# Kernel optimization log

Measured on AMD Instinct MI355X. Metric: run time of the kernel, lower is better.

The kernel has to match this reference:

```python
import jax, jax.numpy as jnp
import numpy as np

EPS = 1e-4
IN_DIM, D1, D2 = 30, 20, 15


def _orthogonal(key, rows, cols):
    # mimic nn.init.orthogonal_ for a (rows, cols) matrix with rows < cols
    a = jax.random.normal(key, (cols, rows), dtype=jnp.float32)
    q, _ = jnp.linalg.qr(a)  # (cols, rows) with orthonormal columns
    return q.T  # (rows, cols), rows orthonormal


def setup_inputs() -> dict:
    key = jax.random.key(0)
    kx, k1, k2 = jax.random.split(key, 3)
    X = jax.random.normal(kx, (65536, IN_DIM, IN_DIM), dtype=jnp.float32)
    W1 = _orthogonal(k1, D1, IN_DIM)
    W2 = _orthogonal(k2, D2, D1)
    return {"X": X, "W1": W1, "W2": W2}


def _bimap(X, W):
    # W @ X @ W^T, symmetrized, + eps*I  -> (b, out, out)
    Y = jnp.einsum('oi,bij,pj->bop', W, X, W)
    Y = (Y + jnp.swapaxes(Y, -1, -2)) * 0.5
    return Y + EPS * jnp.eye(W.shape[0], dtype=Y.dtype)


def _reeig(X):
    w, v = jnp.linalg.eigh(X)
    w = jnp.maximum(w, EPS)
    return jnp.einsum('bik,bk,bjk->bij', v, w, v)


def _logeig(X):
    w, v = jnp.linalg.eigh(X)
    w = jnp.log(jnp.maximum(w, EPS))
    return jnp.einsum('bik,bk,bjk->bij', v, w, v)


def reference(X, W1, W2):
    X = _reeig(_bimap(X, W1))            # (b, 20, 20)
    X = _logeig(_reeig(_bimap(X, W2)))   # (b, 15, 15)
    iu0, iu1 = jnp.triu_indices(D2)      # row-major upper-tri, matches torch.triu_indices
    return X[:, iu0, iu1]                # (b, 120)
```

## Files before the change

### kernel.cpp

```cpp
#include <hip/hip_runtime.h>

#define EPSV 1e-4f

__device__ __forceinline__ float bperm(int addr4, float v) {
  return __int_as_float(__builtin_amdgcn_ds_bpermute(addr4, __float_as_int(v)));
}

template<int N>
__device__ __forceinline__ float selN(const float (&a)[N], int idx) {
  float r = a[0];
#pragma unroll
  for (int k = 1; k < N; ++k) r = (idx == k) ? a[k] : r;
  return r;
}

template<int N>
__device__ void jacobi_eig(float (&a)[N], float (&v)[N], int l, int base4,
                           bool laneValid, float tolsq, int maxSweeps)
{
  constexpr int NH = N / 2;
  const int partner = N - 1 - l;
  const int pslot = (l < NH) ? l : partner;
  const int qslot = N - 1 - pslot;
  const int p4 = base4 + 4 * pslot;
  const int q4 = base4 + 4 * qslot;
  const int pr4 = base4 + 4 * partner;
  const int srcl = (l == 0) ? 0 : ((l == 1) ? (N - 1) : (l - 1));
  const int src4 = base4 + 4 * srcl;
  const bool isP = (l < NH);

  float dval = selN<N>(a, l);
  int sweep = 0;
  while (true) {
    float offAcc = 0.0f;
    for (int r = 0; r < N - 1; ++r) {
      float anti = selN<N>(a, partner);
      float app = bperm(p4, dval);
      float aqq = bperm(q4, dval);
      float apq = bperm(p4, anti);

      float absq = fabsf(apq);
      bool ok = absq > 1e-28f;
      float apqs = ok ? apq : 1.0f;
      float theta = 0.5f * (aqq - app) / apqs;
      float tt = 1.0f / (fabsf(theta) + sqrtf(theta * theta + 1.0f));
      tt = (theta < 0.0f) ? -tt : tt;
      tt = ok ? tt : 0.0f;
      float c = 1.0f / sqrtf(tt * tt + 1.0f);
      float s = tt * c;
      offAcc += laneValid ? apq * apq : 0.0f;

      float seff = isP ? -s : s;
#pragma unroll
      for (int k = 0; k < N; ++k) {
        float pc = bperm(pr4, a[k]);
        a[k] = c * a[k] + seff * pc;
      }
#pragma unroll
      for (int i = 0; i < NH; ++i) {
        float ci = bperm(base4 + 4 * i, c);
        float si = bperm(base4 + 4 * i, s);
        float x = a[i], y = a[N - 1 - i];
        a[i]         = ci * x - si * y;
        a[N - 1 - i] = si * x + ci * y;
        float xv = v[i], yv = v[N - 1 - i];
        v[i]         = ci * xv - si * yv;
        v[N - 1 - i] = si * xv + ci * yv;
      }
      float dnew = isP ? (app - tt * apq) : (aqq + tt * apq);

      float tmp[N];
#pragma unroll
      for (int k = 0; k < N; ++k) tmp[k] = bperm(src4, a[k]);
      a[0] = tmp[0];
      a[1] = tmp[N - 1];
#pragma unroll
      for (int k = 2; k < N; ++k) a[k] = tmp[k - 1];
      float xl = v[N - 1];
#pragma unroll
      for (int k = N - 1; k >= 2; --k) v[k] = v[k - 1];
      v[1] = xl;
      dval = bperm(src4, dnew);
    }
    ++sweep;
#pragma unroll
    for (int m = 1; m < 64; m <<= 1) offAcc += __shfl_xor(offAcc, m);
    if (sweep >= maxSweeps || offAcc < tolsq) break;
  }
}

__global__ __launch_bounds__(256, 3)
void spdnet_kernel(const float* __restrict__ X, const float* __restrict__ W1g,
                   const float* __restrict__ W2g, float* __restrict__ out,
                   int nBatch)
{
  __shared__ __align__(16) float sW1[20 * 32];
  __shared__ __align__(16) float sW2[15 * 20];
  __shared__ __align__(16) float sS[4 * 3 * 964];

  const int tid = threadIdx.x;
  const int wave = tid >> 6;
  const int lane = tid & 63;
  const int grp = lane / 20;
  const int l = lane - grp * 20;
  const int g3 = (grp < 3) ? grp : 2;
  const bool activeG = (grp < 3);
  const int wstart = blockIdx.x * 12 + wave * 3;
  const int bm = wstart + g3;
  const bool valid = activeG && (bm < nBatch);
  const int base4 = g3 * 80;
  float* sSw = sS + wave * (3 * 964);
  float* Sm = sSw + g3 * 964;

  for (int i = tid; i < 600; i += 256) sW1[(i / 30) * 32 + (i % 30)] = W1g[i];
  for (int i = tid; i < 300; i += 256) sW2[i] = W2g[i];

  int nm = nBatch - wstart; nm = nm < 0 ? 0 : (nm > 3 ? 3 : nm);
  const float* Xg = X + (size_t)wstart * 900;
  for (int idx = lane; idx < nm * 900; idx += 64) {
    int m = idx / 900;
    int rem = idx - m * 900;
    int r = rem / 30;
    int kk = rem - r * 30;
    sSw[m * 964 + r * 32 + kk] = Xg[idx];
  }
  __syncthreads();

  for (int t0 = lane; t0 < 2700; t0 += 64) {
    int m = t0 / 900;
    int rem = t0 - m * 900;
    int i = rem / 30;
    int j = rem - i * 30;
    if (i < j && m < nm) {
      float* Sp = sSw + m * 964;
      float x = Sp[i * 32 + j], y = Sp[j * 32 + i];
      float h = 0.5f * (x + y);
      Sp[i * 32 + j] = h;
      Sp[j * 32 + i] = h;
    }
  }
  __syncthreads();

  float w1r[30];
  {
    const float2* wr = (const float2*)(W1g + l * 30);
#pragma unroll
    for (int k2 = 0; k2 < 15; ++k2) {
      float2 q = wr[k2];
      w1r[2 * k2] = q.x; w1r[2 * k2 + 1] = q.y;
    }
  }
  float tcol[30];
#pragma unroll
  for (int r = 0; r < 30; ++r) {
    const float* row = Sm + r * 32;
    const float4* row4 = (const float4*)row;
    float acc = 0.0f;
#pragma unroll
    for (int k4 = 0; k4 < 7; ++k4) {
      float4 q = row4[k4];
      acc += q.x * w1r[4 * k4] + q.y * w1r[4 * k4 + 1] +
             q.z * w1r[4 * k4 + 2] + q.w * w1r[4 * k4 + 3];
    }
    acc += row[28] * w1r[28] + row[29] * w1r[29];
    tcol[r] = acc;
  }
  float a[20], v[20];
#pragma unroll
  for (int i = 0; i < 20; ++i) {
    const float* wrow = sW1 + i * 32;
    const float4* w4 = (const float4*)wrow;
    float acc = 0.0f;
#pragma unroll
    for (int k4 = 0; k4 < 7; ++k4) {
      float4 q = w4[k4];
      acc += q.x * tcol[4 * k4] + q.y * tcol[4 * k4 + 1] +
             q.z * tcol[4 * k4 + 2] + q.w * tcol[4 * k4 + 3];
    }
    acc += wrow[28] * tcol[28] + wrow[29] * tcol[29];
    a[i] = acc + ((i == l) ? EPSV : 0.0f);
    v[i] = (i == l) ? 1.0f : 0.0f;
  }

  jacobi_eig<20>(a, v, l, base4, valid, 2.0e-9f, 12);

  float lam1 = selN<20>(a, l);
  float gs = sqrtf(fmaxf(lam1, EPSV));

  float* Vl = Sm;
  if (activeG) {
#pragma unroll
    for (int k = 0; k < 20; ++k) Vl[l * 21 + k] = v[k];
  }
  __syncthreads();
  float vcol[20];
#pragma unroll
  for (int r = 0; r < 20; ++r) vcol[r] = Vl[r * 21 + l];
  float* Ut = Sm + 448;
  float b[15];
#pragma unroll
  for (int i = 0; i < 15; ++i) {
    const float4* w2r = (const float4*)(sW2 + i * 20);
    float acc = 0.0f;
#pragma unroll
    for (int r4 = 0; r4 < 5; ++r4) {
      float4 q = w2r[r4];
      acc += q.x * vcol[4 * r4] + q.y * vcol[4 * r4 + 1] +
             q.z * vcol[4 * r4 + 2] + q.w * vcol[4 * r4 + 3];
    }
    b[i] = acc;
  }
  if (activeG) {
#pragma unroll
    for (int i = 0; i < 15; ++i) Ut[i * 20 + l] = gs * b[i];
  }
  __syncthreads();

  const int l2 = l & 15;
  float myrow[20];
  {
    const float4* mr = (const float4*)(Ut + ((l2 < 15) ? l2 : 0) * 20);
    float msk = (l2 < 15) ? 1.0f : 0.0f;
#pragma unroll
    for (int r4 = 0; r4 < 5; ++r4) {
      float4 q = mr[r4];
      myrow[4 * r4]     = q.x * msk; myrow[4 * r4 + 1] = q.y * msk;
      myrow[4 * r4 + 2] = q.z * msk; myrow[4 * r4 + 3] = q.w * msk;
    }
  }
  float a2[16], v2[16];
  a2[15] = 0.0f;
#pragma unroll
  for (int r = 0; r < 15; ++r) {
    const float4* ur = (const float4*)(Ut + r * 20);
    float acc = 0.0f;
#pragma unroll
    for (int r4 = 0; r4 < 5; ++r4) {
      float4 q = ur[r4];
      acc += q.x * myrow[4 * r4] + q.y * myrow[4 * r4 + 1] +
             q.z * myrow[4 * r4 + 2] + q.w * myrow[4 * r4 + 3];
    }
    a2[r] = acc + ((r == l2) ? EPSV : 0.0f);
  }
#pragma unroll
  for (int k = 0; k < 16; ++k) v2[k] = (k == l2) ? 1.0f : 0.0f;

  jacobi_eig<16>(a2, v2, l2, base4, valid && (l < 16), 3.0e-10f, 12);

  float lam2 = selN<16>(a2, l2);
  float h = logf(fmaxf(lam2, EPSV));

  __syncthreads();
  float* Wl = Sm;
  float* hl = Sm + 768;
  if (activeG && l < 16) {
#pragma unroll
    for (int k = 0; k < 16; ++k) Wl[l2 * 20 + k] = v2[k];
    hl[l2] = h;
  }
  __syncthreads();

  if (valid && l < 15) {
    float wj[15], hw[15];
#pragma unroll
    for (int k = 0; k < 15; ++k) wj[k] = Wl[l * 20 + k];
#pragma unroll
    for (int k = 0; k < 15; ++k) hw[k] = hl[k] * wj[k];
    float* og = out + (size_t)bm * 120;
#pragma unroll
    for (int i = 0; i < 15; ++i) {
      const float* wr = Wl + i * 20;
      float acc = 0.0f;
#pragma unroll
      for (int k = 0; k < 15; ++k) acc += hw[k] * wr[k];
      if (i <= l) og[15 * i - (i * (i - 1)) / 2 + (l - i)] = acc;
    }
  }
}

extern "C" void kernel_launch(void* const* d_in, const int* in_sizes, int n_in,
                              void* d_out, int out_size, void* d_ws, size_t ws_size,
                              hipStream_t stream) {
  const float* X  = (const float*)d_in[0];
  const float* W1 = (const float*)d_in[1];
  const float* W2 = (const float*)d_in[2];
  float* out = (float*)d_out;
  int nBatch = in_sizes[0] / 900;
  int nBlocks = (nBatch + 11) / 12;
  spdnet_kernel<<<nBlocks, 256, 0, stream>>>(X, W1, W2, out, nBatch);
}
```

Baseline: 4.414 ms.

## Pack eigvec state as float2, halve LDS staging, replace syncs with fences

Several changes land together. The Jacobi state is packed as float2 (a, v) pairs so rotations use packed FMAs, and the division and sqrt calls become rsqrt-based forms. X is staged into LDS in two half-matrix chunks, with symmetrisation folded into the first bimap product, which cuts the per-wave LDS footprint and lets launch bounds rise from 3 to 5 blocks per SM. Most block-wide __syncthreads become __threadfence_block, which relies on each wave touching only its own LDS region, and output is staged in LDS for coalesced stores. The rsqrt-based reciprocal and the changed threshold may alter numerical accuracy, and the register limit may cause spills.

```diff
diff --git a/kernel.cpp b/kernel.cpp
--- a/kernel.cpp
+++ b/kernel.cpp
@@ -1,22 +1,25 @@
 #include <hip/hip_runtime.h>
 
 #define EPSV 1e-4f
+#define REG 484
+
+typedef float v2f __attribute__((ext_vector_type(2)));
 
 __device__ __forceinline__ float bperm(int addr4, float v) {
   return __int_as_float(__builtin_amdgcn_ds_bpermute(addr4, __float_as_int(v)));
 }
 
 template<int N>
-__device__ __forceinline__ float selN(const float (&a)[N], int idx) {
-  float r = a[0];
-#pragma unroll
-  for (int k = 1; k < N; ++k) r = (idx == k) ? a[k] : r;
+__device__ __forceinline__ float selNx(const v2f (&a)[N], int idx) {
+  float r = a[0].x;
+#pragma unroll
+  for (int k = 1; k < N; ++k) r = (idx == k) ? a[k].x : r;
   return r;
 }
 
 template<int N>
-__device__ void jacobi_eig(float (&a)[N], float (&v)[N], int l, int base4,
-                           bool laneValid, float tolsq, int maxSweeps)
+__device__ void jacobi_eig(v2f (&av)[N], int l, int base4, bool laneValid,
+                           float tolsq, int maxSweeps)
 {
   constexpr int NH = N / 2;
   const int partner = N - 1 - l;
@@ -29,57 +32,60 @@
   const int src4 = base4 + 4 * srcl;
   const bool isP = (l < NH);
 
-  float dval = selN<N>(a, l);
+  float dval = selNx<N>(av, l);
   int sweep = 0;
   while (true) {
     float offAcc = 0.0f;
     for (int r = 0; r < N - 1; ++r) {
-      float anti = selN<N>(a, partner);
+      float anti = selNx<N>(av, partner);
       float app = bperm(p4, dval);
       float aqq = bperm(q4, dval);
       float apq = bperm(p4, anti);
 
-      float absq = fabsf(apq);
-      bool ok = absq > 1e-28f;
+      bool ok = fabsf(apq) > 1e-18f;
       float apqs = ok ? apq : 1.0f;
-      float theta = 0.5f * (aqq - app) / apqs;
-      float tt = 1.0f / (fabsf(theta) + sqrtf(theta * theta + 1.0f));
+      float ir = rsqrtf(apqs * apqs);
+      float inva = apqs * ir * ir;
+      float theta = 0.5f * (aqq - app) * inva;
+      float s2t = fminf(theta * theta + 1.0f, 3.0e38f);
+      float rs = rsqrtf(s2t);
+      float den = fabsf(theta) + s2t * rs;
+      float rd = rsqrtf(den * den);
+      float tt = den * rd * rd;
       tt = (theta < 0.0f) ? -tt : tt;
       tt = ok ? tt : 0.0f;
-      float c = 1.0f / sqrtf(tt * tt + 1.0f);
+      float c = rsqrtf(tt * tt + 1.0f);
       float s = tt * c;
       offAcc += laneValid ? apq * apq : 0.0f;
 
       float seff = isP ? -s : s;
 #pragma unroll
       for (int k = 0; k < N; ++k) {
-        float pc = bperm(pr4, a[k]);
-        a[k] = c * a[k] + seff * pc;
+        float pc = bperm(pr4, av[k].x);
+        av[k].x = fmaf(c, av[k].x, seff * pc);
       }
 #pragma unroll
       for (int i = 0; i < NH; ++i) {
         float ci = bperm(base4 + 4 * i, c);
         float si = bperm(base4 + 4 * i, s);
-        float x = a[i], y = a[N - 1 - i];
-        a[i]         = ci * x - si * y;
-        a[N - 1 - i] = si * x + ci * y;
-        float xv = v[i], yv = v[N - 1 - i];
-        v[i]         = ci * xv - si * yv;
-        v[N - 1 - i] = si * xv + ci * yv;
-      }
-      float dnew = isP ? (app - tt * apq) : (aqq + tt * apq);
-
-      float tmp[N];
-#pragma unroll
-      for (int k = 0; k < N; ++k) tmp[k] = bperm(src4, a[k]);
-      a[0] = tmp[0];
-      a[1] = tmp[N - 1];
-#pragma unroll
-      for (int k = 2; k < N; ++k) a[k] = tmp[k - 1];
-      float xl = v[N - 1];
-#pragma unroll
-      for (int k = N - 1; k >= 2; --k) v[k] = v[k - 1];
-      v[1] = xl;
+        v2f c2 = {ci, ci}, s2 = {si, si};
+        v2f x = av[i], y = av[N - 1 - i];
+        v2f m1 = s2 * y;
+        v2f m2 = s2 * x;
+        av[i]         = __builtin_elementwise_fma(c2, x, -m1);
+        av[N - 1 - i] = __builtin_elementwise_fma(c2, y, m2);
+      }
+      float dnew = isP ? fmaf(-tt, apq, app) : fmaf(tt, apq, aqq);
+
+      v2f t0 = av[N - 1];
+#pragma unroll
+      for (int k = N - 1; k >= 2; --k) {
+        av[k].x = bperm(src4, av[k - 1].x);
+        av[k].y = av[k - 1].y;
+      }
+      av[1].x = bperm(src4, t0.x);
+      av[1].y = t0.y;
+      av[0].x = bperm(src4, av[0].x);
       dval = bperm(src4, dnew);
     }
     ++sweep;
@@ -89,14 +95,14 @@
   }
 }
 
-__global__ __launch_bounds__(256, 3)
+__global__ __launch_bounds__(256, 5)
 void spdnet_kernel(const float* __restrict__ X, const float* __restrict__ W1g,
                    const float* __restrict__ W2g, float* __restrict__ out,
                    int nBatch)
 {
   __shared__ __align__(16) float sW1[20 * 32];
   __shared__ __align__(16) float sW2[15 * 20];
-  __shared__ __align__(16) float sS[4 * 3 * 964];
+  __shared__ __align__(16) float sS[4 * 3 * REG];
 
   const int tid = threadIdx.x;
   const int wave = tid >> 6;
@@ -109,37 +115,14 @@
   const int bm = wstart + g3;
   const bool valid = activeG && (bm < nBatch);
   const int base4 = g3 * 80;
-  float* sSw = sS + wave * (3 * 964);
-  float* Sm = sSw + g3 * 964;
+  float* sSw = sS + wave * (3 * REG);
+  float* Sm = sSw + g3 * REG;
 
   for (int i = tid; i < 600; i += 256) sW1[(i / 30) * 32 + (i % 30)] = W1g[i];
   for (int i = tid; i < 300; i += 256) sW2[i] = W2g[i];
 
   int nm = nBatch - wstart; nm = nm < 0 ? 0 : (nm > 3 ? 3 : nm);
   const float* Xg = X + (size_t)wstart * 900;
-  for (int idx = lane; idx < nm * 900; idx += 64) {
-    int m = idx / 900;
-    int rem = idx - m * 900;
-    int r = rem / 30;
-    int kk = rem - r * 30;
-    sSw[m * 964 + r * 32 + kk] = Xg[idx];
-  }
-  __syncthreads();
-
-  for (int t0 = lane; t0 < 2700; t0 += 64) {
-    int m = t0 / 900;
-    int rem = t0 - m * 900;
-    int i = rem / 30;
-    int j = rem - i * 30;
-    if (i < j && m < nm) {
-      float* Sp = sSw + m * 964;
-      float x = Sp[i * 32 + j], y = Sp[j * 32 + i];
-      float h = 0.5f * (x + y);
-      Sp[i * 32 + j] = h;
-      Sp[j * 32 + i] = h;
-    }
-  }
-  __syncthreads();
 
   float w1r[30];
   {
@@ -150,22 +133,56 @@
       w1r[2 * k2] = q.x; w1r[2 * k2 + 1] = q.y;
     }
   }
-  float tcol[30];
-#pragma unroll
-  for (int r = 0; r < 30; ++r) {
-    const float* row = Sm + r * 32;
-    const float4* row4 = (const float4*)row;
-    float acc = 0.0f;
-#pragma unroll
-    for (int k4 = 0; k4 < 7; ++k4) {
-      float4 q = row4[k4];
-      acc += q.x * w1r[4 * k4] + q.y * w1r[4 * k4 + 1] +
-             q.z * w1r[4 * k4 + 2] + q.w * w1r[4 * k4 + 3];
-    }
-    acc += row[28] * w1r[28] + row[29] * w1r[29];
-    tcol[r] = acc;
-  }
-  float a[20], v[20];
+
+  float t[30];
+#pragma unroll
+  for (int r = 0; r < 30; ++r) t[r] = 0.0f;
+
+#pragma unroll
+  for (int c = 0; c < 2; ++c) {
+    for (int idx = lane; idx < nm * 450; idx += 64) {
+      int m = idx / 450;
+      int rem = idx - m * 450;
+      int rr = rem / 30;
+      int kk = rem - rr * 30;
+      sSw[m * REG + rr * 32 + kk] = Xg[m * 900 + c * 450 + rem];
+    }
+    if (c == 0) __syncthreads();
+    else __threadfence_block();
+
+#pragma unroll
+    for (int rr = 0; rr < 15; ++rr) {
+      const float* row = Sm + rr * 32;
+      const float4* row4 = (const float4*)row;
+      float acc = 0.0f;
+#pragma unroll
+      for (int k4 = 0; k4 < 7; ++k4) {
+        float4 q = row4[k4];
+        acc += q.x * w1r[4 * k4] + q.y * w1r[4 * k4 + 1] +
+               q.z * w1r[4 * k4 + 2] + q.w * w1r[4 * k4 + 3];
+      }
+      acc += row[28] * w1r[28] + row[29] * w1r[29];
+      t[c * 15 + rr] += acc;
+    }
+#pragma unroll
+    for (int kk = 0; kk < 15; ++kk) {
+      float wk = w1r[c * 15 + kk];
+      const float* row = Sm + kk * 32;
+      const float4* row4 = (const float4*)row;
+#pragma unroll
+      for (int r4 = 0; r4 < 7; ++r4) {
+        float4 q = row4[r4];
+        t[4 * r4 + 0] += q.x * wk; t[4 * r4 + 1] += q.y * wk;
+        t[4 * r4 + 2] += q.z * wk; t[4 * r4 + 3] += q.w * wk;
+      }
+      t[28] += row[28] * wk; t[29] += row[29] * wk;
+    }
+    if (c == 0) __threadfence_block();
+  }
+#pragma unroll
+  for (int r = 0; r < 30; ++r) t[r] *= 0.5f;
+
+  v2f av[20];
 #pragma unroll
   for (int i = 0; i < 20; ++i) {
     const float* wrow = sW1 + i * 32;
@@ -174,29 +191,30 @@
 #pragma unroll
     for (int k4 = 0; k4 < 7; ++k4) {
       float4 q = w4[k4];
-      acc += q.x * tcol[4 * k4] + q.y * tcol[4 * k4 + 1] +
-             q.z * tcol[4 * k4 + 2] + q.w * tcol[4 * k4 + 3];
-    }
-    acc += wrow[28] * tcol[28] + wrow[29] * tcol[29];
-    a[i] = acc + ((i == l) ? EPSV : 0.0f);
-    v[i] = (i == l) ? 1.0f : 0.0f;
-  }
-
-  jacobi_eig<20>(a, v, l, base4, valid, 2.0e-9f, 12);
-
-  float lam1 = selN<20>(a, l);
+      acc += q.x * t[4 * k4] + q.y * t[4 * k4 + 1] +
+             q.z * t[4 * k4 + 2] + q.w * t[4 * k4 + 3];
+    }
+    acc += wrow[28] * t[28] + wrow[29] * t[29];
+    av[i].x = acc + ((i == l) ? EPSV : 0.0f);
+    av[i].y = (i == l) ? 1.0f : 0.0f;
+  }
+
+  jacobi_eig<20>(av, l, base4, valid, 2.0e-9f, 12);
+
+  float lam1 = selNx<20>(av, l);
   float gs = sqrtf(fmaxf(lam1, EPSV));
 
   float* Vl = Sm;
+  __threadfence_block();
   if (activeG) {
 #pragma unroll
-    for (int k = 0; k < 20; ++k) Vl[l * 21 + k] = v[k];
-  }
-  __syncthreads();
+    for (int k = 0; k < 20; ++k) Vl[l * 21 + k] = av[k].y;
+  }
+  __threadfence_block();
   float vcol[20];
 #pragma unroll
   for (int r = 0; r < 20; ++r) vcol[r] = Vl[r * 21 + l];
-  float* Ut = Sm + 448;
+
   float b[15];
 #pragma unroll
   for (int i = 0; i < 15; ++i) {
@@ -210,16 +228,17 @@
     }
     b[i] = acc;
   }
+  __threadfence_block();
   if (activeG) {
 #pragma unroll
-    for (int i = 0; i < 15; ++i) Ut[i * 20 + l] = gs * b[i];
-  }
-  __syncthreads();
+    for (int i = 0; i < 15; ++i) Sm[i * 20 + l] = gs * b[i];
+  }
+  __threadfence_block();
 
   const int l2 = l & 15;
   float myrow[20];
   {
-    const float4* mr = (const float4*)(Ut + ((l2 < 15) ? l2 : 0) * 20);
+    const float4* mr = (const float4*)(Sm + ((l2 < 15) ? l2 : 0) * 20);
     float msk = (l2 < 15) ? 1.0f : 0.0f;
 #pragma unroll
     for (int r4 = 0; r4 < 5; ++r4) {
@@ -228,11 +247,10 @@
       myrow[4 * r4 + 2] = q.z * msk; myrow[4 * r4 + 3] = q.w * msk;
     }
   }
-  float a2[16], v2[16];
-  a2[15] = 0.0f;
+  v2f av2[16];
 #pragma unroll
   for (int r = 0; r < 15; ++r) {
-    const float4* ur = (const float4*)(Ut + r * 20);
+    const float4* ur = (const float4*)(Sm + r * 20);
     float acc = 0.0f;
 #pragma unroll
     for (int r4 = 0; r4 < 5; ++r4) {
@@ -240,41 +258,45 @@
       acc += q.x * myrow[4 * r4] + q.y * myrow[4 * r4 + 1] +
              q.z * myrow[4 * r4 + 2] + q.w * myrow[4 * r4 + 3];
     }
-    a2[r] = acc + ((r == l2) ? EPSV : 0.0f);
-  }
-#pragma unroll
-  for (int k = 0; k < 16; ++k) v2[k] = (k == l2) ? 1.0f : 0.0f;
-
-  jacobi_eig<16>(a2, v2, l2, base4, valid && (l < 16), 3.0e-10f, 12);
-
-  float lam2 = selN<16>(a2, l2);
+    av2[r].x = acc + ((r == l2) ? EPSV : 0.0f);
+    av2[r].y = (r == l2) ? 1.0f : 0.0f;
+  }
+  av2[15].x = 0.0f;
+  av2[15].y = (l2 == 15) ? 1.0f : 0.0f;
+
+  jacobi_eig<16>(av2, l2, base4, valid && (l < 16), 3.0e-10f, 12);
+
+  float lam2 = selNx<16>(av2, l2);
   float h = logf(fmaxf(lam2, EPSV));
 
-  __syncthreads();
-  float* Wl = Sm;
-  float* hl = Sm + 768;
+  __threadfence_block();
   if (activeG && l < 16) {
 #pragma unroll
-    for (int k = 0; k < 16; ++k) Wl[l2 * 20 + k] = v2[k];
-    hl[l2] = h;
-  }
-  __syncthreads();
-
-  if (valid && l < 15) {
-    float wj[15], hw[15];
-#pragma unroll
-    for (int k = 0; k < 15; ++k) wj[k] = Wl[l * 20 + k];
-#pragma unroll
-    for (int k = 0; k < 15; ++k) hw[k] = hl[k] * wj[k];
-    float* og = out + (size_t)bm * 120;
+    for (int k = 0; k < 16; ++k) Sm[l2 * 20 + k] = av2[k].y;
+    Sm[320 + l2] = h;
+  }
+  __threadfence_block();
+
+  if (activeG && l < 15) {
+    float hw[15];
+#pragma unroll
+    for (int k = 0; k < 15; ++k) hw[k] = Sm[320 + k] * Sm[l * 20 + k];
 #pragma unroll
     for (int i = 0; i < 15; ++i) {
-      const float* wr = Wl + i * 20;
+      const float* wr = Sm + i * 20;
       float acc = 0.0f;
 #pragma unroll
       for (int k = 0; k < 15; ++k) acc += hw[k] * wr[k];
-      if (i <= l) og[15 * i - (i * (i - 1)) / 2 + (l - i)] = acc;
-    }
+      if (i <= l) Sm[336 + 15 * i - (i * (i - 1)) / 2 + (l - i)] = acc;
+    }
+  }
+  __threadfence_block();
+
+  float* og = out + (size_t)wstart * 120;
+  for (int idx = lane; idx < nm * 120; idx += 64) {
+    int m = idx / 120;
+    int off = idx - m * 120;
+    og[idx] = sSw[m * REG + 336 + off];
   }
 }
 
```

Result: slower. 6.021 ms (+36.4%).
